# Performance work log

Measured on AMD Instinct MI355X. Metric: run time of the kernel, lower is better.

Reference implementation:

```python
import jax, jax.numpy as jnp
import numpy as np

N_NODES = 50000
N_EDGES = 800000
IN_FEAT = 128
H_FEAT = 64
NUM_HEADS = 4
NEG_SLOPE = 0.2  # DGL GATConv default LeakyReLU slope


def _gat_conv(feat, src, dst, W, attn_l, attn_r, bias, num_heads, out_feats):
    # feat: [N, Din]; W: [Din, H*F]; attn_l/attn_r: [H, F]; bias: [H*F]
    N = feat.shape[0]
    h = (feat @ W).reshape(N, num_heads, out_feats)          # [N, H, F]
    el = jnp.sum(h * attn_l, axis=-1)                        # [N, H]
    er = jnp.sum(h * attn_r, axis=-1)                        # [N, H]
    e = jax.nn.leaky_relu(el[src] + er[dst], NEG_SLOPE)      # [E, H]
    # segment softmax over incoming edges of each destination node
    m = jax.ops.segment_max(e, dst, num_segments=N)          # [N, H]
    ex = jnp.exp(e - m[dst])                                 # [E, H]
    s = jax.ops.segment_sum(ex, dst, num_segments=N)         # [N, H]
    alpha = ex / s[dst]                                      # [E, H]
    # attn_drop omitted (eval-mode deterministic reference)
    msg = h[src] * alpha[:, :, None]                         # [E, H, F]
    out = jax.ops.segment_sum(msg, dst, num_segments=N)      # [N, H, F]
    return out + bias.reshape(1, num_heads, out_feats)


def setup_inputs() -> dict:
    key = jax.random.key(0)
    ks = jax.random.split(key, 16)
    feat = jax.random.normal(ks[0], (N_NODES, IN_FEAT), dtype=jnp.float32)
    src = jax.random.randint(ks[1], (N_EDGES,), 0, N_NODES)
    dst = jax.random.randint(ks[2], (N_EDGES,), 0, N_NODES)
    sc = 0.1
    H, F = NUM_HEADS, H_FEAT
    params = {
        'W1': jax.random.normal(ks[3], (IN_FEAT, H * F), dtype=jnp.float32) * sc,
        'al1': jax.random.normal(ks[4], (H, F), dtype=jnp.float32) * sc,
        'ar1': jax.random.normal(ks[5], (H, F), dtype=jnp.float32) * sc,
        'b1': jnp.zeros((H * F,), dtype=jnp.float32),
        'W2': jax.random.normal(ks[6], (H * F, H * F), dtype=jnp.float32) * sc,
        'al2': jax.random.normal(ks[7], (H, F), dtype=jnp.float32) * sc,
        'ar2': jax.random.normal(ks[8], (H, F), dtype=jnp.float32) * sc,
        'b2': jnp.zeros((H * F,), dtype=jnp.float32),
        'W3': jax.random.normal(ks[9], (H * F, F), dtype=jnp.float32) * sc,
        'al3': jax.random.normal(ks[10], (1, F), dtype=jnp.float32) * sc,
        'ar3': jax.random.normal(ks[11], (1, F), dtype=jnp.float32) * sc,
        'b3': jnp.zeros((F,), dtype=jnp.float32),
    }
    return {'feat': feat, 'src': src, 'dst': dst, **params}


def reference(feat, src, dst, W1, al1, ar1, b1, W2, al2, ar2, b2, W3, al3, ar3, b3):
    h = _gat_conv(feat, src, dst, W1, al1, ar1, b1, NUM_HEADS, H_FEAT)
    h = jax.nn.relu(h.reshape(h.shape[0], -1))               # flatten(1) + relu
    h = _gat_conv(h, src, dst, W2, al2, ar2, b2, NUM_HEADS, H_FEAT)
    h = jax.nn.relu(h.reshape(h.shape[0], -1))
    h = _gat_conv(h, src, dst, W3, al3, ar3, b3, 1, H_FEAT)
    return h.mean(axis=1)                                    # [N, h_feat]
```

## Files before the change

kernel.cpp:

```cpp
#include <hip/hip_runtime.h>
#include <math.h>

#define N_NODES 50000
#define N_EDGES 800000

typedef short bf8 __attribute__((ext_vector_type(8)));
typedef float f4x __attribute__((ext_vector_type(4)));
typedef float f2v __attribute__((ext_vector_type(2)));
typedef unsigned short us8 __attribute__((ext_vector_type(8)));

__device__ __forceinline__ unsigned short f2bf(float x) {
  unsigned u = __float_as_uint(x);
  unsigned r = (u + 0x7fff + ((u >> 16) & 1)) >> 16;
  return (unsigned short)r;
}
__device__ __forceinline__ float bf2f(unsigned short b) {
  return __uint_as_float(((unsigned)b) << 16);
}
__device__ __forceinline__ f2v bfpair(unsigned d) {
  f2v r;
  r.x = __uint_as_float(d << 16);
  r.y = __uint_as_float(d & 0xffff0000u);
  return r;
}

__device__ __forceinline__ void wt_cvt_one(const float* __restrict__ W,
                                           unsigned short* __restrict__ WT,
                                           int K, int M, int j) {
  int k8n = K >> 3;
  int m = j / k8n, k8 = j - m * k8n;
  us8 o;
#pragma unroll
  for (int r = 0; r < 8; ++r) o[r] = f2bf(W[(size_t)(k8 * 8 + r) * M + m]);
  *(us8*)(WT + (size_t)m * K + k8 * 8) = o;
}

__global__ __launch_bounds__(256) void cvt_all_k(
    const float* __restrict__ feat, unsigned short* __restrict__ featb,
    const float* __restrict__ W1, unsigned short* __restrict__ wt1,
    const float* __restrict__ W2, unsigned short* __restrict__ wt2,
    const float* __restrict__ W3, unsigned short* __restrict__ wt3) {
  const int F8 = N_NODES * 128 / 8;
  int i = blockIdx.x * 256 + threadIdx.x;
  if (i < F8) {
    float4 a = ((const float4*)feat)[2 * i];
    float4 b = ((const float4*)feat)[2 * i + 1];
    us8 o;
    o[0] = f2bf(a.x); o[1] = f2bf(a.y); o[2] = f2bf(a.z); o[3] = f2bf(a.w);
    o[4] = f2bf(b.x); o[5] = f2bf(b.y); o[6] = f2bf(b.z); o[7] = f2bf(b.w);
    ((us8*)featb)[i] = o;
    return;
  }
  int j = i - F8;
  if (j < 4096) {
    wt_cvt_one(W1, wt1, 128, 256, j);
    return;
  }
  j -= 4096;
  if (j < 8192) {
    wt_cvt_one(W2, wt2, 256, 256, j);
    return;
  }
  j -= 8192;
  if (j < 2048) {
    wt_cvt_one(W3, wt3, 256, 64, j);
  }
}

template <int NCT>
__global__ __launch_bounds__(256) void gemm_mfma_k(
    const unsigned short* __restrict__ Xb,
    const unsigned short* __restrict__ WT, unsigned short* __restrict__ Yb,
    float* __restrict__ el, float* __restrict__ er,
    const float* __restrict__ al, const float* __restrict__ ar, int N,
    int K) {
  const int M = NCT * 16;
  const int H = NCT >> 2;
  __shared__ unsigned short As[64][40];
  __shared__ unsigned short Bs[NCT * 16][40];
  const int tile_n = blockIdx.x * 64;
  const int t = threadIdx.x;
  const int wave = t >> 6, lane = t & 63;
  const int quad = lane >> 4, l16 = lane & 15;

  f4x acc[NCT];
#pragma unroll
  for (int ct = 0; ct < NCT; ++ct) acc[ct] = (f4x){0.f, 0.f, 0.f, 0.f};

  const int arow = t >> 2;
  const int akoff = (t & 3) * 8;

  for (int k0 = 0; k0 < K; k0 += 32) {
    {
      int gr = tile_n + arow;
      us8 a = (us8)0;
      if (gr < N) a = *(const us8*)(Xb + (size_t)gr * K + k0 + akoff);
      *(us8*)&As[arow][akoff] = a;
    }
#pragma unroll
    for (int u = 0; u < NCT / 4; ++u) {
      int g = t + u * 256;
      int brow = g >> 2, bk = (g & 3) * 8;
      *(us8*)&Bs[brow][bk] = *(const us8*)(WT + (size_t)brow * K + k0 + bk);
    }
    __syncthreads();
    bf8 afrag = *(const bf8*)&As[wave * 16 + l16][quad * 8];
#pragma unroll
    for (int ct = 0; ct < NCT; ++ct) {
      bf8 bfrag = *(const bf8*)&Bs[ct * 16 + l16][quad * 8];
      acc[ct] = __builtin_amdgcn_mfma_f32_16x16x32_bf16(afrag, bfrag, acc[ct],
                                                        0, 0, 0);
    }
    __syncthreads();
  }
  float al4[NCT], ar4[NCT];
#pragma unroll
  for (int ct = 0; ct < NCT; ++ct) {
    al4[ct] = al[ct * 16 + l16];
    ar4[ct] = ar[ct * 16 + l16];
  }
#pragma unroll
  for (int r = 0; r < 4; ++r) {
    int row = tile_n + wave * 16 + quad * 4 + r;
    float pl[H], pr[H];
#pragma unroll
    for (int h = 0; h < H; ++h) {
      pl[h] = 0.f;
      pr[h] = 0.f;
    }
#pragma unroll
    for (int ct = 0; ct < NCT; ++ct) {
      float y = acc[ct][r];
      pl[ct >> 2] += y * al4[ct];
      pr[ct >> 2] += y * ar4[ct];
      if (row < N) Yb[(size_t)row * M + ct * 16 + l16] = f2bf(y);
    }
#pragma unroll
    for (int off = 1; off < 16; off <<= 1)
#pragma unroll
      for (int h = 0; h < H; ++h) {
        pl[h] += __shfl_xor(pl[h], off);
        pr[h] += __shfl_xor(pr[h], off);
      }
    if (l16 == 0 && row < N) {
#pragma unroll
      for (int h = 0; h < H; ++h) {
        el[row * H + h] = pl[h];
        er[row * H + h] = pr[h];
      }
    }
  }
}

__global__ __launch_bounds__(256) void count_deg_k(
    const int4* __restrict__ dst4, int* __restrict__ deg, int E4) {
  int i = blockIdx.x * blockDim.x + threadIdx.x;
  if (i < E4) {
    int4 d = dst4[i];
    atomicAdd(&deg[d.x], 1);
    atomicAdd(&deg[d.y], 1);
    atomicAdd(&deg[d.z], 1);
    atomicAdd(&deg[d.w], 1);
  }
}

__global__ __launch_bounds__(256) void alloc_rows_k(
    const int* __restrict__ deg, int* __restrict__ rowstart,
    int* __restrict__ cursor, int* __restrict__ gcounter, int N) {
  int i = blockIdx.x * blockDim.x + threadIdx.x;
  int lane = threadIdx.x & 63;
  int d = (i < N) ? deg[i] : 0;
  int x = d;
#pragma unroll
  for (int off = 1; off < 64; off <<= 1) {
    int t = __shfl_up(x, off);
    if (lane >= off) x += t;
  }
  int wsum = __shfl(x, 63);
  int base = 0;
  if (lane == 63) base = atomicAdd(gcounter, wsum);
  base = __shfl(base, 63);
  if (i < N) {
    int mystart = base + x - d;
    rowstart[i] = mystart;
    cursor[i] = mystart;
  }
}

__global__ __launch_bounds__(256) void scatter_k(
    const int4* __restrict__ src4, const int4* __restrict__ dst4,
    int* __restrict__ cursor, int* __restrict__ src_sorted, int E4) {
  int i = blockIdx.x * blockDim.x + threadIdx.x;
  if (i < E4) {
    int4 s = src4[i];
    int4 d = dst4[i];
    int p0 = atomicAdd(&cursor[d.x], 1);
    src_sorted[p0] = s.x;
    int p1 = atomicAdd(&cursor[d.y], 1);
    src_sorted[p1] = s.y;
    int p2 = atomicAdd(&cursor[d.z], 1);
    src_sorted[p2] = s.z;
    int p3 = atomicAdd(&cursor[d.w], 1);
    src_sorted[p3] = s.w;
  }
}

template <int RELU>
__global__ __launch_bounds__(256) void node_agg4_k(
    const unsigned short* __restrict__ hb, const float* __restrict__ el,
    const float* __restrict__ er, const int* __restrict__ rowstart,
    const int* __restrict__ rowend, const int* __restrict__ src_sorted,
    const float* __restrict__ bias, unsigned short* __restrict__ outb,
    int N) {
  int node = blockIdx.x * 4 + (threadIdx.x >> 6);
  int lane = threadIdx.x & 63;
  if (node >= N) return;
  int start = rowstart[node], end = rowend[node];
  int e16 = lane & 15;
  int headA = lane >> 4;
  int eslot = lane >> 5;
  int flane = lane & 31;
  int fo8 = flane << 3;
  int headf = fo8 >> 6;
  float er_a = er[node * 4 + headA];
  f2v acc2[4];
#pragma unroll
  for (int q = 0; q < 4; ++q) acc2[q] = (f2v){0.f, 0.f};
  float ssum = 0.f;
  for (int c0 = start; c0 < end; c0 += 16) {
    int p = c0 + e16;
    bool v = p < end;
    int s = v ? src_sorted[p] : 0;
    float e = el[s * 4 + headA] + er_a;
    e = (e >= 0.f) ? e : 0.2f * e;
    float ex = v ? __expf(e) : 0.f;
    ssum += ex;
    int sjv[8];
    float ajv[8];
#pragma unroll
    for (int jj = 0; jj < 8; ++jj) {
      int idx = (2 * jj + eslot) | (headf << 4);
      sjv[jj] = __shfl(s, idx);
      ajv[jj] = __shfl(ex, idx);
    }
    int nch = end - c0;
    if (nch > 16) nch = 16;
    int nj = (nch + 1) >> 1;
#pragma unroll 8
    for (int jj = 0; jj < nj; ++jj) {
      uint4 d = *(const uint4*)(hb + (size_t)sjv[jj] * 256 + fo8);
      f2v a2 = (f2v){ajv[jj], ajv[jj]};
      acc2[0] += bfpair(d.x) * a2;
      acc2[1] += bfpair(d.y) * a2;
      acc2[2] += bfpair(d.z) * a2;
      acc2[3] += bfpair(d.w) * a2;
    }
  }
#pragma unroll
  for (int off = 1; off < 16; off <<= 1) ssum += __shfl_xor(ssum, off);
  float sden = __shfl(ssum, headf << 4);
  float acc[8];
#pragma unroll
  for (int q = 0; q < 4; ++q) {
    acc[2 * q] = acc2[q].x;
    acc[2 * q + 1] = acc2[q].y;
  }
#pragma unroll
  for (int q = 0; q < 8; ++q) acc[q] += __shfl_xor(acc[q], 32);
  float inv = (end > start) ? 1.f / sden : 0.f;
  if (eslot == 0) {
    us8 o;
#pragma unroll
    for (int q = 0; q < 8; ++q) {
      float vv = acc[q] * inv + bias[fo8 + q];
      if (RELU) vv = fmaxf(vv, 0.f);
      o[q] = f2bf(vv);
    }
    *(us8*)(outb + (size_t)node * 256 + fo8) = o;
  }
}

__global__ __launch_bounds__(256) void node_agg1_k(
    const unsigned short* __restrict__ hb, const float* __restrict__ el,
    const float* __restrict__ er, const int* __restrict__ rowstart,
    const int* __restrict__ rowend, const int* __restrict__ src_sorted,
    const float* __restrict__ bias, float* __restrict__ out, int N) {
  int node = blockIdx.x * 4 + (threadIdx.x >> 6);
  int lane = threadIdx.x & 63;
  if (node >= N) return;
  int start = rowstart[node], end = rowend[node];
  int eslot = lane >> 3;
  int fo8 = (lane & 7) << 3;
  float er_v = er[node];
  f2v acc2[4];
#pragma unroll
  for (int q = 0; q < 4; ++q) acc2[q] = (f2v){0.f, 0.f};
  float ssum = 0.f;
  for (int c0 = start; c0 < end; c0 += 64) {
    int p = c0 + lane;
    bool v = p < end;
    int s = v ? src_sorted[p] : 0;
    float e = el[s] + er_v;
    e = (e >= 0.f) ? e : 0.2f * e;
    float ex = v ? __expf(e) : 0.f;
    ssum += ex;
    int nch = end - c0;
    if (nch > 64) nch = 64;
    int nj = (nch + 7) >> 3;
#pragma unroll 8
    for (int jj = 0; jj < nj; ++jj) {
      int idx = jj * 8 + eslot;
      int sj = __shfl(s, idx);
      float aj = __shfl(ex, idx);
      uint4 d = *(const uint4*)(hb + (size_t)sj * 64 + fo8);
      f2v a2 = (f2v){aj, aj};
      acc2[0] += bfpair(d.x) * a2;
      acc2[1] += bfpair(d.y) * a2;
      acc2[2] += bfpair(d.z) * a2;
      acc2[3] += bfpair(d.w) * a2;
    }
  }
#pragma unroll
  for (int off = 1; off < 64; off <<= 1) ssum += __shfl_xor(ssum, off);
  float acc[8];
#pragma unroll
  for (int q = 0; q < 4; ++q) {
    acc[2 * q] = acc2[q].x;
    acc[2 * q + 1] = acc2[q].y;
  }
#pragma unroll
  for (int off = 8; off < 64; off <<= 1)
#pragma unroll
    for (int q = 0; q < 8; ++q) acc[q] += __shfl_xor(acc[q], off);
  float inv = (end > start) ? 1.f / ssum : 0.f;
  if (eslot == 0) {
    float* o = out + (size_t)node * 64 + fo8;
#pragma unroll
    for (int q = 0; q < 8; ++q) o[q] = acc[q] * inv + bias[fo8 + q];
  }
}

extern "C" void kernel_launch(void* const* d_in, const int* in_sizes, int n_in,
                              void* d_out, int out_size, void* d_ws,
                              size_t ws_size, hipStream_t stream) {
  const float* feat = (const float*)d_in[0];
  const int* src = (const int*)d_in[1];
  const int* dst = (const int*)d_in[2];
  const float* W1 = (const float*)d_in[3];
  const float* al1 = (const float*)d_in[4];
  const float* ar1 = (const float*)d_in[5];
  const float* b1 = (const float*)d_in[6];
  const float* W2 = (const float*)d_in[7];
  const float* al2 = (const float*)d_in[8];
  const float* ar2 = (const float*)d_in[9];
  const float* b2 = (const float*)d_in[10];
  const float* W3 = (const float*)d_in[11];
  const float* al3 = (const float*)d_in[12];
  const float* ar3 = (const float*)d_in[13];
  const float* b3 = (const float*)d_in[14];
  float* out = (float*)d_out;

  unsigned short* hb = (unsigned short*)d_ws;
  unsigned short* fb = hb + (size_t)N_NODES * 256;
  float* el = (float*)(fb + (size_t)N_NODES * 256);
  float* er = el + (size_t)N_NODES * 4;
  int* rowstart = (int*)(er + (size_t)N_NODES * 4);
  int* cursor = rowstart + N_NODES;
  int* deg = cursor + N_NODES;
  int* gcounter = deg + N_NODES;
  int* src_sorted = gcounter + 1;
  unsigned short* wt1 = (unsigned short*)(src_sorted + N_EDGES);
  unsigned short* wt2 = wt1 + 256 * 128;
  unsigned short* wt3 = wt2 + 256 * 256;
  unsigned short* featb = fb;

  const int N = N_NODES, E = N_EDGES;
  const int E4 = E / 4;
  const int GX = (N + 63) / 64;

  const int CVT_TOTAL = N * 128 / 8 + 4096 + 8192 + 2048;
  hipLaunchKernelGGL(cvt_all_k, dim3((CVT_TOTAL + 255) / 256), dim3(256), 0,
                     stream, feat, featb, W1, wt1, W2, wt2, W3, wt3);

  hipMemsetAsync(deg, 0, (size_t)(N + 1) * sizeof(int), stream);
  hipLaunchKernelGGL(count_deg_k, dim3((E4 + 255) / 256), dim3(256), 0, stream,
                     (const int4*)dst, deg, E4);
  hipLaunchKernelGGL(alloc_rows_k, dim3((N + 255) / 256), dim3(256), 0, stream,
                     deg, rowstart, cursor, gcounter, N);
  hipLaunchKernelGGL(scatter_k, dim3((E4 + 255) / 256), dim3(256), 0, stream,
                     (const int4*)src, (const int4*)dst, cursor, src_sorted,
                     E4);

  hipLaunchKernelGGL((gemm_mfma_k<16>), dim3(GX), dim3(256), 0, stream, featb,
                     wt1, hb, el, er, al1, ar1, N, 128);
  hipLaunchKernelGGL((node_agg4_k<1>), dim3((N + 3) / 4), dim3(256), 0, stream,
                     hb, el, er, rowstart, cursor, src_sorted, b1, fb, N);

  hipLaunchKernelGGL((gemm_mfma_k<16>), dim3(GX), dim3(256), 0, stream, fb,
                     wt2, hb, el, er, al2, ar2, N, 256);
  hipLaunchKernelGGL((node_agg4_k<1>), dim3((N + 3) / 4), dim3(256), 0, stream,
                     hb, el, er, rowstart, cursor, src_sorted, b2, fb, N);

  hipLaunchKernelGGL((gemm_mfma_k<4>), dim3(GX), dim3(256), 0, stream, fb, wt3,
                     hb, el, er, al3, ar3, N, 256);
  hipLaunchKernelGGL(node_agg1_k, dim3((N + 3) / 4), dim3(256), 0, stream, hb,
                     el, er, rowstart, cursor, src_sorted, b3, out, N);
}
```

Measured before the change: 426.1 us.

## Store node features in 32-column slices and split aggregation per slice

Node feature matrices (featb, hb, fb) move from row-major [N][256] to a sliced layout [K/32][N][32]. The GEMM reads and writes the sliced layout, and each aggregation block now handles one 32-feature slice for 4 nodes, so grids are 8x (or 2x) larger. The goal is a smaller per-slice gather working set that fits better in cache, but each edge's softmax weights are recomputed in every slice and gathers become 64-byte rows per slice, adding redundant exp and index work.

```diff
diff --git a/kernel.cpp b/kernel.cpp
--- a/kernel.cpp
+++ b/kernel.cpp
@@ -23,6 +23,7 @@
   r.y = __uint_as_float(d & 0xffff0000u);
   return r;
 }
+
 
 __device__ __forceinline__ void wt_cvt_one(const float* __restrict__ W,
                                            unsigned short* __restrict__ WT,
@@ -43,12 +44,13 @@
   const int F8 = N_NODES * 128 / 8;
   int i = blockIdx.x * 256 + threadIdx.x;
   if (i < F8) {
+    int n = i >> 4, c8 = i & 15;
     float4 a = ((const float4*)feat)[2 * i];
     float4 b = ((const float4*)feat)[2 * i + 1];
     us8 o;
     o[0] = f2bf(a.x); o[1] = f2bf(a.y); o[2] = f2bf(a.z); o[3] = f2bf(a.w);
     o[4] = f2bf(b.x); o[5] = f2bf(b.y); o[6] = f2bf(b.z); o[7] = f2bf(b.w);
-    ((us8*)featb)[i] = o;
+    *(us8*)(featb + ((size_t)(c8 >> 2) * N_NODES + n) * 32 + (c8 & 3) * 8) = o;
     return;
   }
   int j = i - F8;
@@ -74,7 +76,6 @@
     float* __restrict__ el, float* __restrict__ er,
     const float* __restrict__ al, const float* __restrict__ ar, int N,
     int K) {
-  const int M = NCT * 16;
   const int H = NCT >> 2;
   __shared__ unsigned short As[64][40];
   __shared__ unsigned short Bs[NCT * 16][40];
@@ -94,7 +95,8 @@
     {
       int gr = tile_n + arow;
       us8 a = (us8)0;
-      if (gr < N) a = *(const us8*)(Xb + (size_t)gr * K + k0 + akoff);
+      if (gr < N)
+        a = *(const us8*)(Xb + ((size_t)(k0 >> 5) * N + gr) * 32 + akoff);
       *(us8*)&As[arow][akoff] = a;
     }
 #pragma unroll
@@ -133,7 +135,8 @@
       float y = acc[ct][r];
       pl[ct >> 2] += y * al4[ct];
       pr[ct >> 2] += y * ar4[ct];
-      if (row < N) Yb[(size_t)row * M + ct * 16 + l16] = f2bf(y);
+      if (row < N)
+        Yb[((size_t)(ct >> 1) * N + row) * 32 + (ct & 1) * 16 + l16] = f2bf(y);
     }
 #pragma unroll
     for (int off = 1; off < 16; off <<= 1)
@@ -206,50 +209,45 @@
 }
 
 template <int RELU>
-__global__ __launch_bounds__(256) void node_agg4_k(
+__global__ __launch_bounds__(256) void node_agg4s_k(
     const unsigned short* __restrict__ hb, const float* __restrict__ el,
     const float* __restrict__ er, const int* __restrict__ rowstart,
     const int* __restrict__ rowend, const int* __restrict__ src_sorted,
     const float* __restrict__ bias, unsigned short* __restrict__ outb,
     int N) {
-  int node = blockIdx.x * 4 + (threadIdx.x >> 6);
-  int lane = threadIdx.x & 63;
+  const int bid = blockIdx.x;
+  const int slice = bid & 7;
+  const int node = (bid >> 3) * 4 + (threadIdx.x >> 6);
+  const int lane = threadIdx.x & 63;
   if (node >= N) return;
+  const int head = slice >> 1;
+  const int flane = lane & 3;
+  const int eslot = lane >> 2;
   int start = rowstart[node], end = rowend[node];
-  int e16 = lane & 15;
-  int headA = lane >> 4;
-  int eslot = lane >> 5;
-  int flane = lane & 31;
-  int fo8 = flane << 3;
-  int headf = fo8 >> 6;
-  float er_a = er[node * 4 + headA];
+  float er_a = er[node * 4 + head];
   f2v acc2[4];
 #pragma unroll
   for (int q = 0; q < 4; ++q) acc2[q] = (f2v){0.f, 0.f};
   float ssum = 0.f;
-  for (int c0 = start; c0 < end; c0 += 16) {
-    int p = c0 + e16;
+  const unsigned short* hslice = hb + (size_t)slice * N * 32;
+  for (int c0 = start; c0 < end; c0 += 64) {
+    int p = c0 + lane;
     bool v = p < end;
     int s = v ? src_sorted[p] : 0;
-    float e = el[s * 4 + headA] + er_a;
+    float e = el[s * 4 + head] + er_a;
     e = (e >= 0.f) ? e : 0.2f * e;
     float ex = v ? __expf(e) : 0.f;
     ssum += ex;
-    int sjv[8];
-    float ajv[8];
-#pragma unroll
-    for (int jj = 0; jj < 8; ++jj) {
-      int idx = (2 * jj + eslot) | (headf << 4);
-      sjv[jj] = __shfl(s, idx);
-      ajv[jj] = __shfl(ex, idx);
-    }
     int nch = end - c0;
-    if (nch > 16) nch = 16;
-    int nj = (nch + 1) >> 1;
-#pragma unroll 8
+    if (nch > 64) nch = 64;
+    int nj = (nch + 15) >> 4;
+#pragma unroll 4
     for (int jj = 0; jj < nj; ++jj) {
-      uint4 d = *(const uint4*)(hb + (size_t)sjv[jj] * 256 + fo8);
-      f2v a2 = (f2v){ajv[jj], ajv[jj]};
+      int idx = jj * 16 + eslot;
+      int sj = __shfl(s, idx);
+      float aj = __shfl(ex, idx);
+      uint4 d = *(const uint4*)(hslice + (size_t)sj * 32 + flane * 8);
+      f2v a2 = (f2v){aj, aj};
       acc2[0] += bfpair(d.x) * a2;
       acc2[1] += bfpair(d.y) * a2;
       acc2[2] += bfpair(d.z) * a2;
@@ -257,8 +255,7 @@
     }
   }
 #pragma unroll
-  for (int off = 1; off < 16; off <<= 1) ssum += __shfl_xor(ssum, off);
-  float sden = __shfl(ssum, headf << 4);
+  for (int off = 1; off < 64; off <<= 1) ssum += __shfl_xor(ssum, off);
   float acc[8];
 #pragma unroll
   for (int q = 0; q < 4; ++q) {
@@ -266,36 +263,41 @@
     acc[2 * q + 1] = acc2[q].y;
   }
 #pragma unroll
-  for (int q = 0; q < 8; ++q) acc[q] += __shfl_xor(acc[q], 32);
-  float inv = (end > start) ? 1.f / sden : 0.f;
+  for (int off = 4; off < 64; off <<= 1)
+#pragma unroll
+    for (int q = 0; q < 8; ++q) acc[q] += __shfl_xor(acc[q], off);
+  float inv = (end > start) ? 1.f / ssum : 0.f;
   if (eslot == 0) {
     us8 o;
 #pragma unroll
     for (int q = 0; q < 8; ++q) {
-      float vv = acc[q] * inv + bias[fo8 + q];
+      float vv = acc[q] * inv + bias[slice * 32 + flane * 8 + q];
       if (RELU) vv = fmaxf(vv, 0.f);
       o[q] = f2bf(vv);
     }
-    *(us8*)(outb + (size_t)node * 256 + fo8) = o;
-  }
-}
-
-__global__ __launch_bounds__(256) void node_agg1_k(
+    *(us8*)(outb + ((size_t)slice * N + node) * 32 + flane * 8) = o;
+  }
+}
+
+__global__ __launch_bounds__(256) void node_agg1s_k(
     const unsigned short* __restrict__ hb, const float* __restrict__ el,
     const float* __restrict__ er, const int* __restrict__ rowstart,
     const int* __restrict__ rowend, const int* __restrict__ src_sorted,
     const float* __restrict__ bias, float* __restrict__ out, int N) {
-  int node = blockIdx.x * 4 + (threadIdx.x >> 6);
-  int lane = threadIdx.x & 63;
+  const int bid = blockIdx.x;
+  const int slice = bid & 1;
+  const int node = (bid >> 1) * 4 + (threadIdx.x >> 6);
+  const int lane = threadIdx.x & 63;
   if (node >= N) return;
+  const int flane = lane & 3;
+  const int eslot = lane >> 2;
   int start = rowstart[node], end = rowend[node];
-  int eslot = lane >> 3;
-  int fo8 = (lane & 7) << 3;
   float er_v = er[node];
   f2v acc2[4];
 #pragma unroll
   for (int q = 0; q < 4; ++q) acc2[q] = (f2v){0.f, 0.f};
   float ssum = 0.f;
+  const unsigned short* hslice = hb + (size_t)slice * N * 32;
   for (int c0 = start; c0 < end; c0 += 64) {
     int p = c0 + lane;
     bool v = p < end;
@@ -306,13 +308,13 @@
     ssum += ex;
     int nch = end - c0;
     if (nch > 64) nch = 64;
-    int nj = (nch + 7) >> 3;
-#pragma unroll 8
+    int nj = (nch + 15) >> 4;
+#pragma unroll 4
     for (int jj = 0; jj < nj; ++jj) {
-      int idx = jj * 8 + eslot;
+      int idx = jj * 16 + eslot;
       int sj = __shfl(s, idx);
       float aj = __shfl(ex, idx);
-      uint4 d = *(const uint4*)(hb + (size_t)sj * 64 + fo8);
+      uint4 d = *(const uint4*)(hslice + (size_t)sj * 32 + flane * 8);
       f2v a2 = (f2v){aj, aj};
       acc2[0] += bfpair(d.x) * a2;
       acc2[1] += bfpair(d.y) * a2;
@@ -329,14 +331,23 @@
     acc[2 * q + 1] = acc2[q].y;
   }
 #pragma unroll
-  for (int off = 8; off < 64; off <<= 1)
+  for (int off = 4; off < 64; off <<= 1)
 #pragma unroll
     for (int q = 0; q < 8; ++q) acc[q] += __shfl_xor(acc[q], off);
   float inv = (end > start) ? 1.f / ssum : 0.f;
   if (eslot == 0) {
-    float* o = out + (size_t)node * 64 + fo8;
-#pragma unroll
-    for (int q = 0; q < 8; ++q) o[q] = acc[q] * inv + bias[fo8 + q];
+    float* o = out + (size_t)node * 64 + slice * 32 + flane * 8;
+    float4 o0, o1;
+    o0.x = acc[0] * inv + bias[slice * 32 + flane * 8 + 0];
+    o0.y = acc[1] * inv + bias[slice * 32 + flane * 8 + 1];
+    o0.z = acc[2] * inv + bias[slice * 32 + flane * 8 + 2];
+    o0.w = acc[3] * inv + bias[slice * 32 + flane * 8 + 3];
+    o1.x = acc[4] * inv + bias[slice * 32 + flane * 8 + 4];
+    o1.y = acc[5] * inv + bias[slice * 32 + flane * 8 + 5];
+    o1.z = acc[6] * inv + bias[slice * 32 + flane * 8 + 6];
+    o1.w = acc[7] * inv + bias[slice * 32 + flane * 8 + 7];
+    *(float4*)(o + 0) = o0;
+    *(float4*)(o + 4) = o1;
   }
 }
 
@@ -377,6 +388,7 @@
   const int N = N_NODES, E = N_EDGES;
   const int E4 = E / 4;
   const int GX = (N + 63) / 64;
+  const int NB4 = ((N + 3) / 4);
 
   const int CVT_TOTAL = N * 128 / 8 + 4096 + 8192 + 2048;
   hipLaunchKernelGGL(cvt_all_k, dim3((CVT_TOTAL + 255) / 256), dim3(256), 0,
@@ -393,16 +405,16 @@
 
   hipLaunchKernelGGL((gemm_mfma_k<16>), dim3(GX), dim3(256), 0, stream, featb,
                      wt1, hb, el, er, al1, ar1, N, 128);
-  hipLaunchKernelGGL((node_agg4_k<1>), dim3((N + 3) / 4), dim3(256), 0, stream,
+  hipLaunchKernelGGL((node_agg4s_k<1>), dim3(NB4 * 8), dim3(256), 0, stream,
                      hb, el, er, rowstart, cursor, src_sorted, b1, fb, N);
 
   hipLaunchKernelGGL((gemm_mfma_k<16>), dim3(GX), dim3(256), 0, stream, fb,
                      wt2, hb, el, er, al2, ar2, N, 256);
-  hipLaunchKernelGGL((node_agg4_k<1>), dim3((N + 3) / 4), dim3(256), 0, stream,
+  hipLaunchKernelGGL((node_agg4s_k<1>), dim3(NB4 * 8), dim3(256), 0, stream,
                      hb, el, er, rowstart, cursor, src_sorted, b2, fb, N);
 
   hipLaunchKernelGGL((gemm_mfma_k<4>), dim3(GX), dim3(256), 0, stream, fb, wt3,
                      hb, el, er, al3, ar3, N, 256);
-  hipLaunchKernelGGL(node_agg1_k, dim3((N + 3) / 4), dim3(256), 0, stream, hb,
-                     el, er, rowstart, cursor, src_sorted, b3, out, N);
-}
+  hipLaunchKernelGGL(node_agg1s_k, dim3(NB4 * 2), dim3(256), 0, stream, hb, el,
+                     er, rowstart, cursor, src_sorted, b3, out, N);
+}
```

After: 672.0 us. +57.7%, slower.
